# Optimization experiments

Measured on AMD Instinct MI355X. Metric: run time of the kernel, lower is better.

Reference implementation:

```python
import jax, jax.numpy as jnp
import numpy as np

N_NODES = 100000
N_EDGES = 1600000
D_IN, D_HID, D_OUT = 128, 128, 64


def setup_inputs() -> dict:
    key = jax.random.key(0)
    k1, k2, k3, k4 = jax.random.split(key, 4)
    x = jax.random.normal(k1, (N_NODES, D_IN), dtype=jnp.float32)
    edge_index = jax.random.randint(k2, (2, N_EDGES), 0, N_NODES, dtype=jnp.int64)
    # Glorot-style weights, zero bias (GCNConv defaults: weight + bias)
    W1 = jax.random.normal(k3, (D_IN, D_HID), dtype=jnp.float32) * (1.0 / np.sqrt(D_IN))
    b1 = jnp.zeros((D_HID,), dtype=jnp.float32)
    W2 = jax.random.normal(k4, (D_HID, D_OUT), dtype=jnp.float32) * (1.0 / np.sqrt(D_HID))
    b2 = jnp.zeros((D_OUT,), dtype=jnp.float32)
    return {"x": x, "edge_index": edge_index, "W1": W1, "b1": b1, "W2": W2, "b2": b2}


def reference(x, edge_index, W1, b1, W2, b2):
    n = x.shape[0]
    src, dst = edge_index[0], edge_index[1]
    # GCN symmetric normalization, add_self_loops=False
    ones = jnp.ones((src.shape[0],), dtype=x.dtype)
    deg = jax.ops.segment_sum(ones, dst, num_segments=n)
    deg_inv_sqrt = jnp.where(deg > 0, jax.lax.rsqrt(jnp.maximum(deg, 1.0)), 0.0)
    norm = deg_inv_sqrt[src] * deg_inv_sqrt[dst]  # [E]

    def gcn_conv(h, W, b):
        h = h @ W                                   # [N, d_out] transform first
        msg = h[src] * norm[:, None]                # [E, d_out] gather + scale
        agg = jax.ops.segment_sum(msg, dst, num_segments=n)  # scatter-add
        return agg + b

    h = jax.nn.relu(gcn_conv(x, W1, b1))
    # dropout(p=0.6) is identity in eval mode (training=False)
    return gcn_conv(h, W2, b2)
```

## Files before the change

### kernel.cpp

```cpp
#include <hip/hip_runtime.h>

#define N_NODES 100000
#define N_EDGES 1600000
#define NBUCK 391
#define CHUNKA 8192
#define NBLKA 196

typedef __bf16 bf16x8 __attribute__((ext_vector_type(8)));
typedef float f32x4 __attribute__((ext_vector_type(4)));

__device__ inline unsigned short bf1(float a) {
    unsigned u = __builtin_bit_cast(unsigned, a);
    u = (u + 0x7FFF + ((u >> 16) & 1)) >> 16;
    return (unsigned short)u;
}
__device__ inline unsigned bfpack(float a, float b) {
    unsigned ua = __builtin_bit_cast(unsigned, a);
    unsigned ub = __builtin_bit_cast(unsigned, b);
    ua = (ua + 0x7FFF + ((ua >> 16) & 1)) >> 16;
    ub = (ub + 0x7FFF + ((ub >> 16) & 1)) >> 16;
    return ua | (ub << 16);
}
__device__ inline float bf2f(unsigned short u) {
    return __builtin_bit_cast(float, ((unsigned)u) << 16);
}
__device__ inline float bflo(unsigned v) { return __builtin_bit_cast(float, v << 16); }
__device__ inline float bfhi(unsigned v) { return __builtin_bit_cast(float, v & 0xFFFF0000u); }

__global__ __launch_bounds__(256) void bhist_kernel(const int* __restrict__ ei,
                                                    int* __restrict__ bhist) {
    __shared__ int hist[NBUCK];
    const int t = threadIdx.x;
    const int e0 = blockIdx.x * CHUNKA;
    const int n  = min(CHUNKA, N_EDGES - e0);
    for (int i = t; i < NBUCK; i += 256) hist[i] = 0;
    __syncthreads();
    for (int i = t; i < n; i += 256) {
        int dst = ei[N_EDGES + e0 + i];
        atomicAdd(&hist[dst >> 8], 1);
    }
    __syncthreads();
    for (int i = t; i < NBUCK; i += 256)
        if (hist[i]) atomicAdd(&bhist[i], hist[i]);
}

__global__ __launch_bounds__(512) void prep_kernel(const int* __restrict__ bhist,
                                                   int* __restrict__ boffs,
                                                   const float* __restrict__ W1,
                                                   const float* __restrict__ W2,
                                                   unsigned short* __restrict__ Wt1,
                                                   unsigned short* __restrict__ Wt2) {
    const int t = threadIdx.x;
    if (blockIdx.x == 0) {
        __shared__ int s[512];
        int v = (t < NBUCK) ? bhist[t] : 0;
        s[t] = v;
        __syncthreads();
#pragma unroll
        for (int off = 1; off < 512; off <<= 1) {
            int tv = (t >= off) ? s[t - off] : 0;
            __syncthreads();
            s[t] += tv;
            __syncthreads();
        }
        if (t < NBUCK) boffs[t] = s[t] - v;
        if (t == NBUCK - 1) boffs[NBUCK] = s[t];
    } else if (blockIdx.x == 1) {
        for (int i = t; i < 128 * 128; i += 512) {
            int k = i >> 7, n = i & 127;
            Wt1[n * 128 + k] = bf1(W1[i]);
        }
    } else {
        for (int i = t; i < 128 * 64; i += 512) {
            int k = i >> 6, n = i & 63;
            Wt2[n * 128 + k] = bf1(W2[i]);
        }
    }
}

__global__ __launch_bounds__(256) void binA_kernel(const int* __restrict__ ei,
                                                   const int* __restrict__ boffs,
                                                   int* __restrict__ bcur,
                                                   unsigned* __restrict__ epk) {
    __shared__ int hist[NBUCK], base[NBUCK], cur[NBUCK];
    const int t = threadIdx.x;
    const int e0 = blockIdx.x * CHUNKA;
    const int n  = min(CHUNKA, N_EDGES - e0);
    for (int i = t; i < NBUCK; i += 256) hist[i] = 0;
    __syncthreads();
    for (int i = t; i < n; i += 256) {
        int dst = ei[N_EDGES + e0 + i];
        atomicAdd(&hist[dst >> 8], 1);
    }
    __syncthreads();
    for (int i = t; i < NBUCK; i += 256) {
        int h = hist[i];
        base[i] = boffs[i] + (h ? atomicAdd(&bcur[i], h) : 0);
        cur[i]  = 0;
    }
    __syncthreads();
    for (int i = t; i < n; i += 256) {
        int src = ei[e0 + i];
        int dst = ei[N_EDGES + e0 + i];
        int b   = dst >> 8;
        int r   = atomicAdd(&cur[b], 1);
        epk[base[b] + r] = ((unsigned)src << 8) | (unsigned)(dst & 255);
    }
}

__global__ __launch_bounds__(256) void binB_kernel(const unsigned* __restrict__ epk,
                                                   const int* __restrict__ boffs,
                                                   int* __restrict__ deg,
                                                   float* __restrict__ dis,
                                                   int* __restrict__ offs,
                                                   int* __restrict__ srcn) {
    __shared__ int cnt[256], s[256], loff[256];
    const int b  = blockIdx.x;
    const int t  = threadIdx.x;
    const int n0 = b << 8;
    const int base = boffs[b];
    const int end  = boffs[b + 1];
    cnt[t] = 0;
    __syncthreads();
    for (int e = base + t; e < end; e += 256)
        atomicAdd(&cnt[epk[e] & 255u], 1);
    __syncthreads();
    int v = cnt[t];
    s[t] = v;
    __syncthreads();
#pragma unroll
    for (int off = 1; off < 256; off <<= 1) {
        int tv = (t >= off) ? s[t - off] : 0;
        __syncthreads();
        s[t] += tv;
        __syncthreads();
    }
    loff[t] = s[t] - v;
    {
        int node = n0 + t;
        if (node < N_NODES) {
            deg[node]  = v;
            dis[node]  = (v > 0) ? rsqrtf((float)v) : 0.0f;
            offs[node] = base + loff[t];
        }
    }
    cnt[t] = 0;
    __syncthreads();
    for (int e = base + t; e < end; e += 256) {
        unsigned p = epk[e];
        int li  = (int)(p & 255u);
        int r   = atomicAdd(&cnt[li], 1);
        srcn[base + loff[li] + r] = (int)(p >> 8);
    }
}

__global__ __launch_bounds__(256) void gemm1_kernel(const float* __restrict__ x,
                                                    const unsigned short* __restrict__ Wt1,
                                                    const float* __restrict__ dis,
                                                    unsigned short* __restrict__ h1b) {
    __shared__ unsigned short Asm[64][136];
    __shared__ float diss[64];
    const int t = threadIdx.x;
    const int node0 = blockIdx.x * 64;

#pragma unroll
    for (int c = 0; c < 4; ++c) {
        int i = c * 256 + t;
        int row = i >> 4, ko = (i & 15) * 8;
        int gn = node0 + row;
        float4 v0 = make_float4(0, 0, 0, 0), v1 = v0;
        if (gn < N_NODES) {
            const float* p = x + (size_t)gn * 128 + ko;
            v0 = *(const float4*)p;
            v1 = *(const float4*)(p + 4);
        }
        uint4 o;
        o.x = bfpack(v0.x, v0.y); o.y = bfpack(v0.z, v0.w);
        o.z = bfpack(v1.x, v1.y); o.w = bfpack(v1.z, v1.w);
        *(uint4*)&Asm[row][ko] = o;
    }
    if (t < 64) {
        int gn = node0 + t;
        diss[t] = (gn < N_NODES) ? dis[gn] : 0.0f;
    }
    __syncthreads();

    const int wv = t >> 6, ln = t & 63;
    const int lc = ln & 15, q = ln >> 4;
    const int n0 = wv * 32;

    bf16x8 bfr[2][4];
#pragma unroll
    for (int nt = 0; nt < 2; ++nt)
#pragma unroll
        for (int k = 0; k < 4; ++k)
            bfr[nt][k] = *(const bf16x8*)(Wt1 + (size_t)(n0 + nt * 16 + lc) * 128 + k * 32 + q * 8);

    f32x4 acc[4][2];
#pragma unroll
    for (int m = 0; m < 4; ++m)
#pragma unroll
        for (int nt = 0; nt < 2; ++nt) acc[m][nt] = (f32x4)(0.0f);

#pragma unroll
    for (int k = 0; k < 4; ++k) {
        bf16x8 af[4];
#pragma unroll
        for (int m = 0; m < 4; ++m)
            af[m] = *(const bf16x8*)&Asm[m * 16 + lc][k * 32 + q * 8];
#pragma unroll
        for (int m = 0; m < 4; ++m)
#pragma unroll
            for (int nt = 0; nt < 2; ++nt)
                acc[m][nt] = __builtin_amdgcn_mfma_f32_16x16x32_bf16(af[m], bfr[nt][k], acc[m][nt], 0, 0, 0);
    }

#pragma unroll
    for (int m = 0; m < 4; ++m)
#pragma unroll
        for (int r = 0; r < 4; ++r) {
            int lr = m * 16 + q * 4 + r;
            int gn = node0 + lr;
            if (gn < N_NODES) {
                float dv = diss[lr];
#pragma unroll
                for (int nt = 0; nt < 2; ++nt)
                    h1b[(size_t)gn * 128 + n0 + nt * 16 + lc] = bf1(acc[m][nt][r] * dv);
            }
        }
}

__global__ __launch_bounds__(256) void agg1gemm2_kernel(const int* __restrict__ srcn,
                                                        const int* __restrict__ offs,
                                                        const int* __restrict__ deg,
                                                        const float* __restrict__ dis,
                                                        const unsigned short* __restrict__ h1b,
                                                        const float* __restrict__ b1,
                                                        const unsigned short* __restrict__ Wt2,
                                                        unsigned short* __restrict__ h2b) {
    __shared__ unsigned short Zs[64][136];
    __shared__ float diss[64];
    __shared__ int offs_s[64], deg_s[64];
    const int t = threadIdx.x;
    const int node0 = blockIdx.x * 64;
    if (t < 64) {
        int gn = node0 + t;
        bool ok = gn < N_NODES;
        offs_s[t] = ok ? offs[gn] : 0;
        deg_s[t]  = ok ? deg[gn] : 0;
        diss[t]   = ok ? dis[gn] : 0.0f;
    }
    __syncthreads();

    const int wv = t >> 6, ln = t & 63;
    const int qw = ln >> 4, lc = ln & 15;
    const uint4* __restrict__ h1q = (const uint4*)h1b;

    float4 bbA = *(const float4*)(b1 + lc * 8);
    float4 bbB = *(const float4*)(b1 + lc * 8 + 4);

#define ACC8(v)                                    \
    do {                                           \
        f0 += bflo((v).x); f1 += bfhi((v).x);      \
        f2 += bflo((v).y); f3 += bfhi((v).y);      \
        f4 += bflo((v).z); f5 += bfhi((v).z);      \
        f6 += bflo((v).w); f7 += bfhi((v).w);      \
    } while (0)

    for (int r = 0; r < 4; ++r) {
        const int lr  = wv * 16 + r * 4 + qw;
        const int beg = offs_s[lr];
        const int d   = deg_s[lr];
        float f0 = 0.f, f1 = 0.f, f2 = 0.f, f3 = 0.f,
              f4 = 0.f, f5 = 0.f, f6 = 0.f, f7 = 0.f;
        int k = 0;
        for (; k + 4 <= d; k += 4) {
            int s0 = srcn[beg + k];
            int s1 = srcn[beg + k + 1];
            int s2 = srcn[beg + k + 2];
            int s3 = srcn[beg + k + 3];
            uint4 v0 = h1q[(size_t)s0 * 16 + lc];
            uint4 v1 = h1q[(size_t)s1 * 16 + lc];
            uint4 v2 = h1q[(size_t)s2 * 16 + lc];
            uint4 v3 = h1q[(size_t)s3 * 16 + lc];
            ACC8(v0); ACC8(v1); ACC8(v2); ACC8(v3);
        }
        for (; k < d; ++k) {
            int s = srcn[beg + k];
            uint4 v = h1q[(size_t)s * 16 + lc];
            ACC8(v);
        }
        float dv = diss[lr];
        uint4 o;
        o.x = bfpack(fmaxf(dv * f0 + bbA.x, 0.0f), fmaxf(dv * f1 + bbA.y, 0.0f));
        o.y = bfpack(fmaxf(dv * f2 + bbA.z, 0.0f), fmaxf(dv * f3 + bbA.w, 0.0f));
        o.z = bfpack(fmaxf(dv * f4 + bbB.x, 0.0f), fmaxf(dv * f5 + bbB.y, 0.0f));
        o.w = bfpack(fmaxf(dv * f6 + bbB.z, 0.0f), fmaxf(dv * f7 + bbB.w, 0.0f));
        *(uint4*)&Zs[lr][lc * 8] = o;
    }
#undef ACC8
    __syncthreads();

    const int lc2 = ln & 15, q = ln >> 4;
    const int n0 = wv * 16;

    bf16x8 bfr[4];
#pragma unroll
    for (int k = 0; k < 4; ++k)
        bfr[k] = *(const bf16x8*)(Wt2 + (size_t)(n0 + lc2) * 128 + k * 32 + q * 8);

    f32x4 acc[4];
#pragma unroll
    for (int m = 0; m < 4; ++m) acc[m] = (f32x4)(0.0f);

#pragma unroll
    for (int k = 0; k < 4; ++k) {
        bf16x8 af[4];
#pragma unroll
        for (int m = 0; m < 4; ++m)
            af[m] = *(const bf16x8*)&Zs[m * 16 + lc2][k * 32 + q * 8];
#pragma unroll
        for (int m = 0; m < 4; ++m)
            acc[m] = __builtin_amdgcn_mfma_f32_16x16x32_bf16(af[m], bfr[k], acc[m], 0, 0, 0);
    }

#pragma unroll
    for (int m = 0; m < 4; ++m)
#pragma unroll
        for (int r = 0; r < 4; ++r) {
            int lr = m * 16 + q * 4 + r;
            int gn = node0 + lr;
            if (gn < N_NODES) {
                float dv = diss[lr];
                h2b[(size_t)gn * 64 + n0 + lc2] = bf1(acc[m][r] * dv);
            }
        }
}

__global__ __launch_bounds__(256) void agg2_kernel(const int* __restrict__ srcn,
                                                   const int* __restrict__ offs,
                                                   const int* __restrict__ deg,
                                                   const float* __restrict__ dis,
                                                   const unsigned short* __restrict__ h2b,
                                                   const float* __restrict__ b2,
                                                   float* __restrict__ out) {
    __shared__ float diss[64];
    __shared__ int offs_s[64], deg_s[64];
    const int t = threadIdx.x;
    const int node0 = blockIdx.x * 64;
    if (t < 64) {
        int gn = node0 + t;
        bool ok = gn < N_NODES;
        offs_s[t] = ok ? offs[gn] : 0;
        deg_s[t]  = ok ? deg[gn] : 0;
        diss[t]   = ok ? dis[gn] : 0.0f;
    }
    __syncthreads();

    const int wv = t >> 6, ln = t & 63;
    const int qw = ln >> 4, lc = ln & 15;
    const uint2* __restrict__ h2v = (const uint2*)h2b;

    float4 bb = *(const float4*)(b2 + lc * 4);

#define ACC4(v)                                    \
    do {                                           \
        f0 += bflo((v).x); f1 += bfhi((v).x);      \
        f2 += bflo((v).y); f3 += bfhi((v).y);      \
    } while (0)

    for (int r = 0; r < 4; ++r) {
        const int lr  = wv * 16 + r * 4 + qw;
        const int beg = offs_s[lr];
        const int d   = deg_s[lr];
        float f0 = 0.f, f1 = 0.f, f2 = 0.f, f3 = 0.f;
        int k = 0;
        for (; k + 4 <= d; k += 4) {
            int s0 = srcn[beg + k];
            int s1 = srcn[beg + k + 1];
            int s2 = srcn[beg + k + 2];
            int s3 = srcn[beg + k + 3];
            uint2 v0 = h2v[(size_t)s0 * 16 + lc];
            uint2 v1 = h2v[(size_t)s1 * 16 + lc];
            uint2 v2 = h2v[(size_t)s2 * 16 + lc];
            uint2 v3 = h2v[(size_t)s3 * 16 + lc];
            ACC4(v0); ACC4(v1); ACC4(v2); ACC4(v3);
        }
        for (; k < d; ++k) {
            int s = srcn[beg + k];
            uint2 v = h2v[(size_t)s * 16 + lc];
            ACC4(v);
        }
        int gn = node0 + lr;
        if (gn < N_NODES) {
            float dv = diss[lr];
            float4 o;
            o.x = dv * f0 + bb.x;
            o.y = dv * f1 + bb.y;
            o.z = dv * f2 + bb.z;
            o.w = dv * f3 + bb.w;
            *(float4*)(out + (size_t)gn * 64 + lc * 4) = o;
        }
    }
#undef ACC4
}

extern "C" void kernel_launch(void* const* d_in, const int* in_sizes, int n_in,
                              void* d_out, int out_size, void* d_ws, size_t ws_size,
                              hipStream_t stream) {
    const float* x  = (const float*)d_in[0];
    const int*   ei = (const int*)d_in[1];
    const float* W1 = (const float*)d_in[2];
    const float* b1 = (const float*)d_in[3];
    const float* W2 = (const float*)d_in[4];
    const float* b2 = (const float*)d_in[5];
    float* out = (float*)d_out;

    char* ws = (char*)d_ws;
    int*   bhist = (int*)(ws);
    int*   bcur  = (int*)(ws + (size_t)4 * 1024);
    int*   boffs = (int*)(ws + (size_t)8 * 1024);
    int*   deg   = (int*)(ws + (size_t)16 * 1024);
    int*   offs  = (int*)(ws + (size_t)512 * 1024);
    float* dis   = (float*)(ws + (size_t)1024 * 1024);
    unsigned short* Wt1 = (unsigned short*)(ws + (size_t)1536 * 1024);
    unsigned short* Wt2 = (unsigned short*)(ws + (size_t)1600 * 1024);
    unsigned* epk = (unsigned*)(ws + (size_t)2560 * 1024);
    int*   srcn  = (int*)(ws + (size_t)9216 * 1024);
    unsigned short* h1b = (unsigned short*)(ws + (size_t)16 * 1024 * 1024);
    unsigned short* h2b = (unsigned short*)(ws + (size_t)48 * 1024 * 1024);

    hipMemsetAsync(ws, 0, (size_t)8 * 1024, stream);

    bhist_kernel<<<NBLKA, 256, 0, stream>>>(ei, bhist);
    prep_kernel<<<3, 512, 0, stream>>>(bhist, boffs, W1, W2, Wt1, Wt2);
    binA_kernel<<<NBLKA, 256, 0, stream>>>(ei, boffs, bcur, epk);
    binB_kernel<<<NBUCK, 256, 0, stream>>>(epk, boffs, deg, dis, offs, srcn);
    gemm1_kernel<<<(N_NODES + 63) / 64, 256, 0, stream>>>(x, Wt1, dis, h1b);
    agg1gemm2_kernel<<<(N_NODES + 63) / 64, 256, 0, stream>>>(srcn, offs, deg, dis,
                                                              h1b, b1, Wt2, h2b);
    agg2_kernel<<<(N_NODES + 63) / 64, 256, 0, stream>>>(srcn, offs, deg, dis,
                                                         h2b, b2, out);
}
```

Measured before the change: 283.2 us.

## Halve binning chunk size, vectorize edge reads, unroll gathers by eight

Result: faster. 269.3 us (-4.9%).

```diff
diff --git a/kernel.cpp b/kernel.cpp
--- a/kernel.cpp
+++ b/kernel.cpp
@@ -3,8 +3,8 @@
 #define N_NODES 100000
 #define N_EDGES 1600000
 #define NBUCK 391
-#define CHUNKA 8192
-#define NBLKA 196
+#define CHUNKA 4096
+#define NBLKA 391
 
 typedef __bf16 bf16x8 __attribute__((ext_vector_type(8)));
 typedef float f32x4 __attribute__((ext_vector_type(4)));
@@ -21,9 +21,6 @@
     ub = (ub + 0x7FFF + ((ub >> 16) & 1)) >> 16;
     return ua | (ub << 16);
 }
-__device__ inline float bf2f(unsigned short u) {
-    return __builtin_bit_cast(float, ((unsigned)u) << 16);
-}
 __device__ inline float bflo(unsigned v) { return __builtin_bit_cast(float, v << 16); }
 __device__ inline float bfhi(unsigned v) { return __builtin_bit_cast(float, v & 0xFFFF0000u); }
 
@@ -35,9 +32,14 @@
     const int n  = min(CHUNKA, N_EDGES - e0);
     for (int i = t; i < NBUCK; i += 256) hist[i] = 0;
     __syncthreads();
-    for (int i = t; i < n; i += 256) {
-        int dst = ei[N_EDGES + e0 + i];
-        atomicAdd(&hist[dst >> 8], 1);
+    const int4* __restrict__ dst4 = (const int4*)(ei + N_EDGES + e0);
+    const int n4 = n >> 2;
+    for (int i = t; i < n4; i += 256) {
+        int4 d = dst4[i];
+        atomicAdd(&hist[d.x >> 8], 1);
+        atomicAdd(&hist[d.y >> 8], 1);
+        atomicAdd(&hist[d.z >> 8], 1);
+        atomicAdd(&hist[d.w >> 8], 1);
     }
     __syncthreads();
     for (int i = t; i < NBUCK; i += 256)
@@ -86,11 +88,17 @@
     const int t = threadIdx.x;
     const int e0 = blockIdx.x * CHUNKA;
     const int n  = min(CHUNKA, N_EDGES - e0);
+    const int n4 = n >> 2;
+    const int4* __restrict__ src4 = (const int4*)(ei + e0);
+    const int4* __restrict__ dst4 = (const int4*)(ei + N_EDGES + e0);
     for (int i = t; i < NBUCK; i += 256) hist[i] = 0;
     __syncthreads();
-    for (int i = t; i < n; i += 256) {
-        int dst = ei[N_EDGES + e0 + i];
-        atomicAdd(&hist[dst >> 8], 1);
+    for (int i = t; i < n4; i += 256) {
+        int4 d = dst4[i];
+        atomicAdd(&hist[d.x >> 8], 1);
+        atomicAdd(&hist[d.y >> 8], 1);
+        atomicAdd(&hist[d.z >> 8], 1);
+        atomicAdd(&hist[d.w >> 8], 1);
     }
     __syncthreads();
     for (int i = t; i < NBUCK; i += 256) {
@@ -99,12 +107,17 @@
         cur[i]  = 0;
     }
     __syncthreads();
-    for (int i = t; i < n; i += 256) {
-        int src = ei[e0 + i];
-        int dst = ei[N_EDGES + e0 + i];
-        int b   = dst >> 8;
-        int r   = atomicAdd(&cur[b], 1);
-        epk[base[b] + r] = ((unsigned)src << 8) | (unsigned)(dst & 255);
+    for (int i = t; i < n4; i += 256) {
+        int4 s = src4[i];
+        int4 d = dst4[i];
+#define PUT(ss, dd)                                               \
+        do {                                                      \
+            int b = (dd) >> 8;                                    \
+            int r = atomicAdd(&cur[b], 1);                        \
+            epk[base[b] + r] = ((unsigned)(ss) << 8) | (unsigned)((dd) & 255); \
+        } while (0)
+        PUT(s.x, d.x); PUT(s.y, d.y); PUT(s.z, d.z); PUT(s.w, d.w);
+#undef PUT
     }
 }
 
@@ -274,6 +287,26 @@
         float f0 = 0.f, f1 = 0.f, f2 = 0.f, f3 = 0.f,
               f4 = 0.f, f5 = 0.f, f6 = 0.f, f7 = 0.f;
         int k = 0;
+        for (; k + 8 <= d; k += 8) {
+            int s0 = srcn[beg + k];
+            int s1 = srcn[beg + k + 1];
+            int s2 = srcn[beg + k + 2];
+            int s3 = srcn[beg + k + 3];
+            int s4 = srcn[beg + k + 4];
+            int s5 = srcn[beg + k + 5];
+            int s6 = srcn[beg + k + 6];
+            int s7 = srcn[beg + k + 7];
+            uint4 v0 = h1q[(size_t)s0 * 16 + lc];
+            uint4 v1 = h1q[(size_t)s1 * 16 + lc];
+            uint4 v2 = h1q[(size_t)s2 * 16 + lc];
+            uint4 v3 = h1q[(size_t)s3 * 16 + lc];
+            uint4 v4 = h1q[(size_t)s4 * 16 + lc];
+            uint4 v5 = h1q[(size_t)s5 * 16 + lc];
+            uint4 v6 = h1q[(size_t)s6 * 16 + lc];
+            uint4 v7 = h1q[(size_t)s7 * 16 + lc];
+            ACC8(v0); ACC8(v1); ACC8(v2); ACC8(v3);
+            ACC8(v4); ACC8(v5); ACC8(v6); ACC8(v7);
+        }
         for (; k + 4 <= d; k += 4) {
             int s0 = srcn[beg + k];
             int s1 = srcn[beg + k + 1];
@@ -375,6 +408,26 @@
         const int d   = deg_s[lr];
         float f0 = 0.f, f1 = 0.f, f2 = 0.f, f3 = 0.f;
         int k = 0;
+        for (; k + 8 <= d; k += 8) {
+            int s0 = srcn[beg + k];
+            int s1 = srcn[beg + k + 1];
+            int s2 = srcn[beg + k + 2];
+            int s3 = srcn[beg + k + 3];
+            int s4 = srcn[beg + k + 4];
+            int s5 = srcn[beg + k + 5];
+            int s6 = srcn[beg + k + 6];
+            int s7 = srcn[beg + k + 7];
+            uint2 v0 = h2v[(size_t)s0 * 16 + lc];
+            uint2 v1 = h2v[(size_t)s1 * 16 + lc];
+            uint2 v2 = h2v[(size_t)s2 * 16 + lc];
+            uint2 v3 = h2v[(size_t)s3 * 16 + lc];
+            uint2 v4 = h2v[(size_t)s4 * 16 + lc];
+            uint2 v5 = h2v[(size_t)s5 * 16 + lc];
+            uint2 v6 = h2v[(size_t)s6 * 16 + lc];
+            uint2 v7 = h2v[(size_t)s7 * 16 + lc];
+            ACC4(v0); ACC4(v1); ACC4(v2); ACC4(v3);
+            ACC4(v4); ACC4(v5); ACC4(v6); ACC4(v7);
+        }
         for (; k + 4 <= d; k += 4) {
             int s0 = srcn[beg + k];
             int s1 = srcn[beg + k + 1];
```
